# Kernel tuning notes

Measured on AMD Instinct MI355X. Metric: run time of the kernel, lower is better.

The kernel has to match this reference:

```python
import jax, jax.numpy as jnp
import numpy as np

N_NODES = 50000
IN_DIM = 128
HID = 128
N_EDGES = 1000000


def setup_inputs() -> dict:
    key = jax.random.key(0)
    k1, k2, k3, k4, k5, k6, k7 = jax.random.split(key, 7)
    patient_embeds = jax.random.normal(k1, (N_NODES, IN_DIM), dtype=jnp.float32)
    condition_embeds = jax.random.normal(k2, (N_NODES, IN_DIM), dtype=jnp.float32)
    edge_index = jax.random.randint(k3, (2, N_EDGES), 0, N_NODES, dtype=jnp.int64)
    # MLP params: Linear(2*IN_DIM -> HID), Linear(HID -> 1)
    s1 = 1.0 / np.sqrt(2 * IN_DIM)
    s2 = 1.0 / np.sqrt(HID)
    W1 = jax.random.uniform(k4, (2 * IN_DIM, HID), minval=-s1, maxval=s1, dtype=jnp.float32)
    b1 = jax.random.uniform(k5, (HID,), minval=-s1, maxval=s1, dtype=jnp.float32)
    W2 = jax.random.uniform(k6, (HID, 1), minval=-s2, maxval=s2, dtype=jnp.float32)
    b2 = jax.random.uniform(k7, (1,), minval=-s2, maxval=s2, dtype=jnp.float32)
    return {
        "patient_embeds": patient_embeds,
        "condition_embeds": condition_embeds,
        "edge_index": edge_index,
        "W1": W1, "b1": b1, "W2": W2, "b2": b2,
    }


def reference(patient_embeds, condition_embeds, edge_index, W1, b1, W2, b2):
    src = patient_embeds[edge_index[0]]        # [E, D]
    dst = condition_embeds[edge_index[1]]      # [E, D]
    # concat + first Linear == split-matmul; avoids materializing [E, 2D]
    h = src @ W1[:IN_DIM] + dst @ W1[IN_DIM:] + b1   # [E, HID]
    h = jax.nn.relu(h)
    logits = h @ W2 + b2                        # [E, 1]
    return jax.nn.sigmoid(logits).squeeze(-1)   # [E]
```

## Files before the change

kernel.cpp:

```cpp
#include <hip/hip_runtime.h>
#include <hip/hip_bf16.h>

#define IN_DIM   128
#define HIDDEN   128
#define KDIM     256
#define TILE_E   32
#define NTHREADS 512
#define LDBW     264

typedef __attribute__((ext_vector_type(8)))  short bf16x8;
typedef __attribute__((ext_vector_type(16))) float f32x16;

__device__ __forceinline__ unsigned short f2bf(float f) {
    union { __hip_bfloat16 h; unsigned short u; } cv;
    cv.h = __float2bfloat16(f);
    return cv.u;
}

__global__ void prep_kernel(const float* __restrict__ pat,
                            const float* __restrict__ cond,
                            const float* __restrict__ W1,
                            unsigned short* __restrict__ pat_bf,
                            unsigned short* __restrict__ cond_bf,
                            unsigned short* __restrict__ W1T,
                            int n_vec, int do_tables) {
    const int w1_units = HIDDEN * KDIM / 8;
    const long long total = do_tables ? (2LL * n_vec + w1_units) : w1_units;
    const long long stride = (long long)gridDim.x * blockDim.x;
    for (long long u = blockIdx.x * (long long)blockDim.x + threadIdx.x;
         u < total; u += stride) {
        if (do_tables && u < 2LL * n_vec) {
            int which = (u >= n_vec);
            long long v = which ? u - n_vec : u;
            const float* src = which ? cond : pat;
            unsigned short* dst = which ? cond_bf : pat_bf;
            long long base = v * 8;
            float4 x = *(const float4*)(src + base);
            float4 y = *(const float4*)(src + base + 4);
            unsigned short hv[8];
            hv[0]=f2bf(x.x); hv[1]=f2bf(x.y); hv[2]=f2bf(x.z); hv[3]=f2bf(x.w);
            hv[4]=f2bf(y.x); hv[5]=f2bf(y.y); hv[6]=f2bf(y.z); hv[7]=f2bf(y.w);
            *(uint4*)(dst + base) = *(uint4*)hv;
        } else {
            int idx = (int)(u - (do_tables ? 2LL * n_vec : 0));
            int c  = idx >> 5;
            int k0 = (idx & 31) * 8;
            unsigned short hv[8];
            #pragma unroll
            for (int j = 0; j < 8; ++j)
                hv[j] = f2bf(W1[(k0 + j) * HIDDEN + c]);
            *(uint4*)(W1T + c * KDIM + k0) = *(uint4*)hv;
        }
    }
}

__global__ __launch_bounds__(NTHREADS, 4)
void link_mlp_kernel(const float* __restrict__ pat,
                     const float* __restrict__ cond,
                     const unsigned short* __restrict__ tbl_p,
                     const unsigned short* __restrict__ tbl_c,
                     const int* __restrict__ eidx,
                     const unsigned short* __restrict__ W1T,
                     const float* __restrict__ b1,
                     const float* __restrict__ W2,
                     const float* __restrict__ b2,
                     float* __restrict__ out,
                     int E, int n_nodes, int ntiles)
{
    __shared__ unsigned short sB[HIDDEN * LDBW];
    __shared__ float sLog[8][TILE_E];

    const int t = threadIdx.x;

    #pragma unroll
    for (int it = 0; it < 8; ++it) {
        int ci = it * NTHREADS + t;
        int c = ci >> 5, j = ci & 31;
        *(uint4*)&sB[c * LDBW + j * 8] = *(const uint4*)(W1T + c * KDIM + j * 8);
    }
    __syncthreads();

    const int w    = t >> 6;
    const int lane = t & 63;
    const int c32  = lane & 31;
    const int hi   = lane >> 5;

    float b1v[4], w2v[4];
    #pragma unroll
    for (int nt = 0; nt < 4; ++nt) {
        int col = nt * 32 + c32;
        b1v[nt] = b1[col];
        w2v[nt] = W2[col];
    }
    const float b2v = b2[0];

    const int wslots = gridDim.x * (NTHREADS / 64);

    for (int tile = blockIdx.x * (NTHREADS / 64) + w; tile < ntiles; tile += wslots) {
        const int e  = tile * TILE_E + c32;
        const int eC = min(e, E - 1);
        int np = eidx[eC];     np = min(max(np, 0), n_nodes - 1);
        int nc = eidx[E + eC]; nc = min(max(nc, 0), n_nodes - 1);

        f32x16 acc[4];
        #pragma unroll
        for (int nt = 0; nt < 4; ++nt)
            acc[nt] = (f32x16){0.f,0.f,0.f,0.f,0.f,0.f,0.f,0.f,
                               0.f,0.f,0.f,0.f,0.f,0.f,0.f,0.f};

        if (tbl_p) {
            const unsigned short* bp = tbl_p + np * IN_DIM + hi * 8;
            const unsigned short* bc = tbl_c + nc * IN_DIM + hi * 8;
            #pragma unroll
            for (int ksb = 0; ksb < 4; ++ksb) {
                bf16x8 a[4];
                #pragma unroll
                for (int j = 0; j < 4; ++j) {
                    int ks = ksb * 4 + j;
                    const unsigned short* src =
                        (ks < 8) ? (bp + ks * 16) : (bc + (ks - 8) * 16);
                    a[j] = *(const bf16x8*)src;
                }
                #pragma unroll
                for (int j = 0; j < 4; ++j) {
                    int ks = ksb * 4 + j;
                    #pragma unroll
                    for (int nt = 0; nt < 4; ++nt) {
                        bf16x8 b = *(const bf16x8*)
                            &sB[(nt * 32 + c32) * LDBW + ks * 16 + hi * 8];
                        acc[nt] = __builtin_amdgcn_mfma_f32_32x32x16_bf16(
                            a[j], b, acc[nt], 0, 0, 0);
                    }
                }
            }
        } else {
            const float* fp = pat  + (long long)np * IN_DIM + hi * 8;
            const float* fc = cond + (long long)nc * IN_DIM + hi * 8;
            #pragma unroll
            for (int ksb = 0; ksb < 4; ++ksb) {
                bf16x8 a[4];
                #pragma unroll
                for (int j = 0; j < 4; ++j) {
                    int ks = ksb * 4 + j;
                    const float* src = (ks < 8) ? (fp + ks * 16) : (fc + (ks - 8) * 16);
                    float4 x = *(const float4*)src;
                    float4 y = *(const float4*)(src + 4);
                    unsigned short hv[8];
                    hv[0]=f2bf(x.x); hv[1]=f2bf(x.y); hv[2]=f2bf(x.z); hv[3]=f2bf(x.w);
                    hv[4]=f2bf(y.x); hv[5]=f2bf(y.y); hv[6]=f2bf(y.z); hv[7]=f2bf(y.w);
                    a[j] = *(bf16x8*)hv;
                }
                #pragma unroll
                for (int j = 0; j < 4; ++j) {
                    int ks = ksb * 4 + j;
                    #pragma unroll
                    for (int nt = 0; nt < 4; ++nt) {
                        bf16x8 b = *(const bf16x8*)
                            &sB[(nt * 32 + c32) * LDBW + ks * 16 + hi * 8];
                        acc[nt] = __builtin_amdgcn_mfma_f32_32x32x16_bf16(
                            a[j], b, acc[nt], 0, 0, 0);
                    }
                }
            }
        }

        float p[16];
        #pragma unroll
        for (int r = 0; r < 16; ++r) {
            float s = 0.f;
            #pragma unroll
            for (int nt = 0; nt < 4; ++nt)
                s += fmaxf(acc[nt][r] + b1v[nt], 0.f) * w2v[nt];
            p[r] = s;
        }
        #pragma unroll
        for (int off = 1; off < 32; off <<= 1)
            #pragma unroll
            for (int r = 0; r < 16; ++r)
                p[r] += __shfl_xor(p[r], off, 64);
        if (c32 == 0) {
            #pragma unroll
            for (int r = 0; r < 16; ++r)
                sLog[w][(r & 3) + 8 * (r >> 2) + 4 * hi] = p[r];
        }
        float x  = sLog[w][c32] + b2v;
        float sg = 1.f / (1.f + __expf(-x));
        if (hi == 0 && e < E) out[e] = sg;
    }
}

extern "C" void kernel_launch(void* const* d_in, const int* in_sizes, int n_in,
                              void* d_out, int out_size, void* d_ws, size_t ws_size,
                              hipStream_t stream) {
    const float* pat  = (const float*)d_in[0];
    const float* cond = (const float*)d_in[1];
    const int*   eidx = (const int*)d_in[2];
    const float* W1   = (const float*)d_in[3];
    const float* b1   = (const float*)d_in[4];
    const float* W2   = (const float*)d_in[5];
    const float* b2   = (const float*)d_in[6];
    float*       out  = (float*)d_out;

    const int E       = in_sizes[2] / 2;
    const int n_nodes = in_sizes[0] / IN_DIM;
    const int ntiles  = (E + TILE_E - 1) / TILE_E;

    unsigned short* W1T = (unsigned short*)d_ws;
    const size_t tbl_bytes = (size_t)n_nodes * IN_DIM * 2;
    unsigned short* pat_bf  = (unsigned short*)((char*)d_ws + 65536);
    unsigned short* cond_bf = (unsigned short*)((char*)d_ws + 65536 + tbl_bytes);
    const bool use_tbl = ws_size >= 65536 + 2 * tbl_bytes;

    const int n_vec = n_nodes * IN_DIM / 8;
    prep_kernel<<<2048, 256, 0, stream>>>(pat, cond, W1, pat_bf, cond_bf, W1T,
                                          n_vec, use_tbl ? 1 : 0);

    const int nblocks = 512;
    link_mlp_kernel<<<nblocks, NTHREADS, 0, stream>>>(
        pat, cond,
        use_tbl ? pat_bf : nullptr, use_tbl ? cond_bf : nullptr,
        eidx, W1T, b1, W2, b2, out, E, n_nodes, ntiles);
}
```

Baseline: 190.7 us.

## Software-pipeline gathers across tiles and use transpose-style shuffle reduction

Splits the bf16-table path into a dedicated kernel that prefetches the next tile's indices and patient rows while the current tile's MFMAs run, so gather latency is overlapped with compute. The cross-lane reduction is replaced with a butterfly that halves the live values at each step and writes outputs directly, removing the shared-memory logit buffer. Launch bounds drop to 2 blocks per CU to give room for the extra registers that hold prefetched fragments, which may lower occupancy.

```diff
diff --git a/kernel.cpp b/kernel.cpp
--- a/kernel.cpp
+++ b/kernel.cpp
@@ -54,10 +54,25 @@
     }
 }
 
-__global__ __launch_bounds__(NTHREADS, 4)
-void link_mlp_kernel(const float* __restrict__ pat,
-                     const float* __restrict__ cond,
-                     const unsigned short* __restrict__ tbl_p,
+#define LOADC(Ab, base, off)                                        \
+    { _Pragma("unroll")                                             \
+      for (int j = 0; j < 4; ++j)                                   \
+          Ab[j] = *(const bf16x8*)((base) + (off) + j * 16); }
+
+#define MFMA_CHUNK(Ab, ks0)                                         \
+    { _Pragma("unroll")                                             \
+      for (int j = 0; j < 4; ++j) {                                 \
+          const int ks = (ks0) + j;                                 \
+          _Pragma("unroll")                                         \
+          for (int nt = 0; nt < 4; ++nt) {                          \
+              bf16x8 bfrag = *(const bf16x8*)                       \
+                  &sB[(nt * 32 + c32) * LDBW + ks * 16 + hi * 8];   \
+              acc[nt] = __builtin_amdgcn_mfma_f32_32x32x16_bf16(    \
+                  Ab[j], bfrag, acc[nt], 0, 0, 0);                  \
+          } } }
+
+__global__ __launch_bounds__(NTHREADS, 2)
+void link_mlp_kernel(const unsigned short* __restrict__ tbl_p,
                      const unsigned short* __restrict__ tbl_c,
                      const int* __restrict__ eidx,
                      const unsigned short* __restrict__ W1T,
@@ -68,10 +83,8 @@
                      int E, int n_nodes, int ntiles)
 {
     __shared__ unsigned short sB[HIDDEN * LDBW];
-    __shared__ float sLog[8][TILE_E];
 
     const int t = threadIdx.x;
-
     #pragma unroll
     for (int it = 0; it < 8; ++it) {
         int ci = it * NTHREADS + t;
@@ -94,6 +107,147 @@
     }
     const float b2v = b2[0];
 
+    const int ws = gridDim.x * (NTHREADS / 64);
+    int tile = blockIdx.x * (NTHREADS / 64) + w;
+    if (tile >= ntiles) return;
+
+    const unsigned short* bcC;
+    bf16x8 A0[4], A1[4], A2[4], A3[4];
+    {
+        int eC = min(tile * TILE_E + c32, E - 1);
+        int npR = eidx[eC], ncR = eidx[E + eC];
+        int np = min(max(npR, 0), n_nodes - 1);
+        int nc = min(max(ncR, 0), n_nodes - 1);
+        const unsigned short* bpC = tbl_p + np * IN_DIM + hi * 8;
+        bcC = tbl_c + nc * IN_DIM + hi * 8;
+        LOADC(A0, bpC, 0);
+        LOADC(A1, bpC, 64);
+    }
+    int npN = 0, ncN = 0;
+    {
+        int tn = tile + ws;
+        if (tn < ntiles) {
+            int e2 = min(tn * TILE_E + c32, E - 1);
+            npN = eidx[e2]; ncN = eidx[E + e2];
+        }
+    }
+
+    while (true) {
+        LOADC(A2, bcC, 0);
+        LOADC(A3, bcC, 64);
+
+        f32x16 acc[4];
+        #pragma unroll
+        for (int nt = 0; nt < 4; ++nt)
+            acc[nt] = (f32x16){0.f,0.f,0.f,0.f,0.f,0.f,0.f,0.f,
+                               0.f,0.f,0.f,0.f,0.f,0.f,0.f,0.f};
+
+        MFMA_CHUNK(A0, 0);
+        MFMA_CHUNK(A1, 4);
+
+        const int tn = tile + ws;
+        const unsigned short* bcN;
+        {
+            int np = min(max(npN, 0), n_nodes - 1);
+            int nc = min(max(ncN, 0), n_nodes - 1);
+            const unsigned short* bpN = tbl_p + np * IN_DIM + hi * 8;
+            bcN = tbl_c + nc * IN_DIM + hi * 8;
+            if (tn < ntiles) {
+                LOADC(A0, bpN, 0);
+                LOADC(A1, bpN, 64);
+                int tnn = min(tn + ws, ntiles - 1);
+                int e3 = min(tnn * TILE_E + c32, E - 1);
+                npN = eidx[e3]; ncN = eidx[E + e3];
+            }
+        }
+
+        MFMA_CHUNK(A2, 8);
+        MFMA_CHUNK(A3, 12);
+
+        float v[16];
+        #pragma unroll
+        for (int r = 0; r < 16; ++r) {
+            float s = 0.f;
+            #pragma unroll
+            for (int nt = 0; nt < 4; ++nt)
+                s += fmaxf(acc[nt][r] + b1v[nt], 0.f) * w2v[nt];
+            v[r] = s;
+        }
+        #pragma unroll
+        for (int j = 0; j < 16; ++j) v[j] += __shfl_xor(v[j], 1, 64);
+        const bool bb0 = (lane & 1);
+        float w8[8];
+        #pragma unroll
+        for (int j = 0; j < 8; ++j) w8[j] = bb0 ? v[j + 8] : v[j];
+        #pragma unroll
+        for (int j = 0; j < 8; ++j) w8[j] += __shfl_xor(w8[j], 2, 64);
+        const bool bb1 = (lane >> 1) & 1;
+        float x4[4];
+        #pragma unroll
+        for (int j = 0; j < 4; ++j) x4[j] = bb1 ? w8[j + 4] : w8[j];
+        #pragma unroll
+        for (int j = 0; j < 4; ++j) x4[j] += __shfl_xor(x4[j], 4, 64);
+        const bool bb2 = (lane >> 2) & 1;
+        float y2[2];
+        #pragma unroll
+        for (int j = 0; j < 2; ++j) y2[j] = bb2 ? x4[j + 2] : x4[j];
+        #pragma unroll
+        for (int j = 0; j < 2; ++j) y2[j] += __shfl_xor(y2[j], 8, 64);
+        const bool bb3 = (lane >> 3) & 1;
+        float z = bb3 ? y2[1] : y2[0];
+        z += __shfl_xor(z, 16, 64);
+
+        {
+            int r = ((lane & 1) << 3) | (((lane >> 1) & 1) << 2) |
+                    (((lane >> 2) & 1) << 1) | ((lane >> 3) & 1);
+            int row = (r & 3) + ((r >> 2) << 3) + 4 * hi;
+            int erow = tile * TILE_E + row;
+            if (!(lane & 16) && erow < E)
+                out[erow] = 1.f / (1.f + __expf(-(z + b2v)));
+        }
+
+        if (tn >= ntiles) break;
+        bcC = bcN;
+        tile = tn;
+    }
+}
+
+__global__ __launch_bounds__(NTHREADS, 2)
+void link_mlp_f32_kernel(const float* __restrict__ pat,
+                         const float* __restrict__ cond,
+                         const int* __restrict__ eidx,
+                         const unsigned short* __restrict__ W1T,
+                         const float* __restrict__ b1,
+                         const float* __restrict__ W2,
+                         const float* __restrict__ b2,
+                         float* __restrict__ out,
+                         int E, int n_nodes, int ntiles)
+{
+    __shared__ unsigned short sB[HIDDEN * LDBW];
+    __shared__ float sLog[8][TILE_E];
+
+    const int t = threadIdx.x;
+    #pragma unroll
+    for (int it = 0; it < 8; ++it) {
+        int ci = it * NTHREADS + t;
+        int c = ci >> 5, j = ci & 31;
+        *(uint4*)&sB[c * LDBW + j * 8] = *(const uint4*)(W1T + c * KDIM + j * 8);
+    }
+    __syncthreads();
+
+    const int w    = t >> 6;
+    const int lane = t & 63;
+    const int c32  = lane & 31;
+    const int hi   = lane >> 5;
+
+    float b1v[4], w2v[4];
+    #pragma unroll
+    for (int nt = 0; nt < 4; ++nt) {
+        int col = nt * 32 + c32;
+        b1v[nt] = b1[col];
+        w2v[nt] = W2[col];
+    }
+    const float b2v = b2[0];
     const int wslots = gridDim.x * (NTHREADS / 64);
 
     for (int tile = blockIdx.x * (NTHREADS / 64) + w; tile < ntiles; tile += wslots) {
@@ -108,58 +262,31 @@
             acc[nt] = (f32x16){0.f,0.f,0.f,0.f,0.f,0.f,0.f,0.f,
                                0.f,0.f,0.f,0.f,0.f,0.f,0.f,0.f};
 
-        if (tbl_p) {
-            const unsigned short* bp = tbl_p + np * IN_DIM + hi * 8;
-            const unsigned short* bc = tbl_c + nc * IN_DIM + hi * 8;
-            #pragma unroll
-            for (int ksb = 0; ksb < 4; ++ksb) {
-                bf16x8 a[4];
+        const float* fp = pat  + (long long)np * IN_DIM + hi * 8;
+        const float* fc = cond + (long long)nc * IN_DIM + hi * 8;
+        #pragma unroll
+        for (int ksb = 0; ksb < 4; ++ksb) {
+            bf16x8 a[4];
+            #pragma unroll
+            for (int j = 0; j < 4; ++j) {
+                int ks = ksb * 4 + j;
+                const float* src = (ks < 8) ? (fp + ks * 16) : (fc + (ks - 8) * 16);
+                float4 x = *(const float4*)src;
+                float4 y = *(const float4*)(src + 4);
+                unsigned short hv[8];
+                hv[0]=f2bf(x.x); hv[1]=f2bf(x.y); hv[2]=f2bf(x.z); hv[3]=f2bf(x.w);
+                hv[4]=f2bf(y.x); hv[5]=f2bf(y.y); hv[6]=f2bf(y.z); hv[7]=f2bf(y.w);
+                a[j] = *(bf16x8*)hv;
+            }
+            #pragma unroll
+            for (int j = 0; j < 4; ++j) {
+                int ks = ksb * 4 + j;
                 #pragma unroll
-                for (int j = 0; j < 4; ++j) {
-                    int ks = ksb * 4 + j;
-                    const unsigned short* src =
-                        (ks < 8) ? (bp + ks * 16) : (bc + (ks - 8) * 16);
-                    a[j] = *(const bf16x8*)src;
-                }
-                #pragma unroll
-                for (int j = 0; j < 4; ++j) {
-                    int ks = ksb * 4 + j;
-                    #pragma unroll
-                    for (int nt = 0; nt < 4; ++nt) {
-                        bf16x8 b = *(const bf16x8*)
-                            &sB[(nt * 32 + c32) * LDBW + ks * 16 + hi * 8];
-                        acc[nt] = __builtin_amdgcn_mfma_f32_32x32x16_bf16(
-                            a[j], b, acc[nt], 0, 0, 0);
-                    }
-                }
-            }
-        } else {
-            const float* fp = pat  + (long long)np * IN_DIM + hi * 8;
-            const float* fc = cond + (long long)nc * IN_DIM + hi * 8;
-            #pragma unroll
-            for (int ksb = 0; ksb < 4; ++ksb) {
-                bf16x8 a[4];
-                #pragma unroll
-                for (int j = 0; j < 4; ++j) {
-                    int ks = ksb * 4 + j;
-                    const float* src = (ks < 8) ? (fp + ks * 16) : (fc + (ks - 8) * 16);
-                    float4 x = *(const float4*)src;
-                    float4 y = *(const float4*)(src + 4);
-                    unsigned short hv[8];
-                    hv[0]=f2bf(x.x); hv[1]=f2bf(x.y); hv[2]=f2bf(x.z); hv[3]=f2bf(x.w);
-                    hv[4]=f2bf(y.x); hv[5]=f2bf(y.y); hv[6]=f2bf(y.z); hv[7]=f2bf(y.w);
-                    a[j] = *(bf16x8*)hv;
-                }
-                #pragma unroll
-                for (int j = 0; j < 4; ++j) {
-                    int ks = ksb * 4 + j;
-                    #pragma unroll
-                    for (int nt = 0; nt < 4; ++nt) {
-                        bf16x8 b = *(const bf16x8*)
-                            &sB[(nt * 32 + c32) * LDBW + ks * 16 + hi * 8];
-                        acc[nt] = __builtin_amdgcn_mfma_f32_32x32x16_bf16(
-                            a[j], b, acc[nt], 0, 0, 0);
-                    }
+                for (int nt = 0; nt < 4; ++nt) {
+                    bf16x8 b = *(const bf16x8*)
+                        &sB[(nt * 32 + c32) * LDBW + ks * 16 + hi * 8];
+                    acc[nt] = __builtin_amdgcn_mfma_f32_32x32x16_bf16(
+                        a[j], b, acc[nt], 0, 0, 0);
                 }
             }
         }
@@ -216,8 +343,11 @@
                                           n_vec, use_tbl ? 1 : 0);
 
     const int nblocks = 512;
-    link_mlp_kernel<<<nblocks, NTHREADS, 0, stream>>>(
-        pat, cond,
-        use_tbl ? pat_bf : nullptr, use_tbl ? cond_bf : nullptr,
-        eidx, W1T, b1, W2, b2, out, E, n_nodes, ntiles);
-}
+    if (use_tbl) {
+        link_mlp_kernel<<<nblocks, NTHREADS, 0, stream>>>(
+            pat_bf, cond_bf, eidx, W1T, b1, W2, b2, out, E, n_nodes, ntiles);
+    } else {
+        link_mlp_f32_kernel<<<nblocks, NTHREADS, 0, stream>>>(
+            pat, cond, eidx, W1T, b1, W2, b2, out, E, n_nodes, ntiles);
+    }
+}
```

New measurement: 473.5 us. 2.48x slower.

## Precompute per-node hidden projections, then gather and sum per edge in slices

Applied to the files above, without the earlier changes.

The first linear layer is split algebraically. Each node's patient and condition rows are projected once through W1 with MFMA into bf16 hidden tables, replacing a 256-deep matmul on every edge. The edge pass then gathers 16-wide slices of the two projected rows, adds them, applies ReLU and a dot with W2, and writes bf16 partial sums per slice; a finalize kernel sums the slices and applies the sigmoid. This cuts the per-edge MFMA work, but adds an intermediate partial-sum buffer, an extra kernel launch, and bf16 rounding of both the hidden values and the partial sums.

```diff
diff --git a/kernel.cpp b/kernel.cpp
--- a/kernel.cpp
+++ b/kernel.cpp
@@ -4,9 +4,10 @@
 #define IN_DIM   128
 #define HIDDEN   128
 #define KDIM     256
-#define TILE_E   32
-#define NTHREADS 512
+#define NTH_G    512
 #define LDBW     264
+#define NSLICE   8
+#define SLICE_D  16
 
 typedef __attribute__((ext_vector_type(8)))  short bf16x8;
 typedef __attribute__((ext_vector_type(16))) float f32x16;
@@ -16,88 +17,199 @@
     cv.h = __float2bfloat16(f);
     return cv.u;
 }
-
-__global__ void prep_kernel(const float* __restrict__ pat,
-                            const float* __restrict__ cond,
-                            const float* __restrict__ W1,
-                            unsigned short* __restrict__ pat_bf,
-                            unsigned short* __restrict__ cond_bf,
-                            unsigned short* __restrict__ W1T,
-                            int n_vec, int do_tables) {
-    const int w1_units = HIDDEN * KDIM / 8;
-    const long long total = do_tables ? (2LL * n_vec + w1_units) : w1_units;
-    const long long stride = (long long)gridDim.x * blockDim.x;
-    for (long long u = blockIdx.x * (long long)blockDim.x + threadIdx.x;
-         u < total; u += stride) {
-        if (do_tables && u < 2LL * n_vec) {
-            int which = (u >= n_vec);
-            long long v = which ? u - n_vec : u;
-            const float* src = which ? cond : pat;
-            unsigned short* dst = which ? cond_bf : pat_bf;
-            long long base = v * 8;
-            float4 x = *(const float4*)(src + base);
-            float4 y = *(const float4*)(src + base + 4);
-            unsigned short hv[8];
-            hv[0]=f2bf(x.x); hv[1]=f2bf(x.y); hv[2]=f2bf(x.z); hv[3]=f2bf(x.w);
-            hv[4]=f2bf(y.x); hv[5]=f2bf(y.y); hv[6]=f2bf(y.z); hv[7]=f2bf(y.w);
-            *(uint4*)(dst + base) = *(uint4*)hv;
-        } else {
-            int idx = (int)(u - (do_tables ? 2LL * n_vec : 0));
-            int c  = idx >> 5;
-            int k0 = (idx & 31) * 8;
-            unsigned short hv[8];
-            #pragma unroll
-            for (int j = 0; j < 8; ++j)
-                hv[j] = f2bf(W1[(k0 + j) * HIDDEN + c]);
-            *(uint4*)(W1T + c * KDIM + k0) = *(uint4*)hv;
-        }
-    }
-}
-
-__global__ __launch_bounds__(NTHREADS, 4)
-void link_mlp_kernel(const float* __restrict__ pat,
-                     const float* __restrict__ cond,
-                     const unsigned short* __restrict__ tbl_p,
-                     const unsigned short* __restrict__ tbl_c,
-                     const int* __restrict__ eidx,
-                     const unsigned short* __restrict__ W1T,
-                     const float* __restrict__ b1,
-                     const float* __restrict__ W2,
-                     const float* __restrict__ b2,
-                     float* __restrict__ out,
-                     int E, int n_nodes, int ntiles)
+__device__ __forceinline__ float bf_lo(unsigned int v) { return __uint_as_float(v << 16); }
+__device__ __forceinline__ float bf_hi(unsigned int v) { return __uint_as_float(v & 0xffff0000u); }
+
+__global__ void w1t_kernel(const float* __restrict__ W1,
+                           unsigned short* __restrict__ W1T) {
+    int o = blockIdx.x * blockDim.x + threadIdx.x;
+    if (o >= HIDDEN * KDIM / 8) return;
+    int c = o >> 5;
+    int k0 = (o & 31) * 8;
+    unsigned short hv[8];
+    #pragma unroll
+    for (int j = 0; j < 8; ++j) hv[j] = f2bf(W1[(k0 + j) * HIDDEN + c]);
+    *(uint4*)(W1T + c * KDIM + k0) = *(uint4*)hv;
+}
+
+__global__ __launch_bounds__(NTH_G, 4)
+void hgemm_kernel(const float* __restrict__ pat,
+                  const float* __restrict__ cond,
+                  const unsigned short* __restrict__ W1T,
+                  const float* __restrict__ b1,
+                  unsigned short* __restrict__ hpS,
+                  unsigned short* __restrict__ hcS,
+                  int n_nodes)
 {
     __shared__ unsigned short sB[HIDDEN * LDBW];
-    __shared__ float sLog[8][TILE_E];
-
     const int t = threadIdx.x;
-
     #pragma unroll
     for (int it = 0; it < 8; ++it) {
-        int ci = it * NTHREADS + t;
+        int ci = it * NTH_G + t;
         int c = ci >> 5, j = ci & 31;
         *(uint4*)&sB[c * LDBW + j * 8] = *(const uint4*)(W1T + c * KDIM + j * 8);
     }
     __syncthreads();
 
-    const int w    = t >> 6;
-    const int lane = t & 63;
-    const int c32  = lane & 31;
-    const int hi   = lane >> 5;
-
-    float b1v[4], w2v[4];
+    const int w = t >> 6, lane = t & 63, c32 = lane & 31, hi = lane >> 5;
+    const int pass = w >> 2;
+    const int m    = w & 3;
+    const int nb   = blockIdx.x * 128 + m * 32;
+    if (nb >= n_nodes) return;
+
+    const float* tbl = pass ? cond : pat;
+    const int row = min(nb + c32, n_nodes - 1);
+
+    bf16x8 A[8];
+    #pragma unroll
+    for (int ks = 0; ks < 8; ++ks) {
+        const float* ap = tbl + (long long)row * IN_DIM + ks * 16 + hi * 8;
+        float4 x = *(const float4*)ap;
+        float4 y = *(const float4*)(ap + 4);
+        unsigned short hv[8];
+        hv[0]=f2bf(x.x); hv[1]=f2bf(x.y); hv[2]=f2bf(x.z); hv[3]=f2bf(x.w);
+        hv[4]=f2bf(y.x); hv[5]=f2bf(y.y); hv[6]=f2bf(y.z); hv[7]=f2bf(y.w);
+        A[ks] = *(bf16x8*)hv;
+    }
+
+    f32x16 acc[4];
+    #pragma unroll
+    for (int nt = 0; nt < 4; ++nt)
+        acc[nt] = (f32x16){0.f,0.f,0.f,0.f,0.f,0.f,0.f,0.f,
+                           0.f,0.f,0.f,0.f,0.f,0.f,0.f,0.f};
+    #pragma unroll
+    for (int ks = 0; ks < 8; ++ks)
+        #pragma unroll
+        for (int nt = 0; nt < 4; ++nt) {
+            bf16x8 b = *(const bf16x8*)
+                &sB[(nt * 32 + c32) * LDBW + pass * 128 + ks * 16 + hi * 8];
+            acc[nt] = __builtin_amdgcn_mfma_f32_32x32x16_bf16(A[ks], b, acc[nt], 0, 0, 0);
+        }
+
+    float b1v[4];
+    #pragma unroll
+    for (int nt = 0; nt < 4; ++nt) b1v[nt] = pass ? 0.f : b1[nt * 32 + c32];
+    unsigned short* dst = pass ? hcS : hpS;
+
     #pragma unroll
     for (int nt = 0; nt < 4; ++nt) {
         int col = nt * 32 + c32;
-        b1v[nt] = b1[col];
-        w2v[nt] = W2[col];
-    }
+        int sl = col >> 4, j = col & 15;
+        unsigned short* dcol = dst + (long long)sl * n_nodes * SLICE_D + j;
+        #pragma unroll
+        for (int r = 0; r < 16; ++r) {
+            int node = nb + (r & 3) + 8 * (r >> 2) + 4 * hi;
+            if (node < n_nodes)
+                dcol[(long long)node * SLICE_D] = f2bf(acc[nt][r] + b1v[nt]);
+        }
+    }
+}
+
+__global__ __launch_bounds__(256, 4)
+void edge_kernel(const unsigned short* __restrict__ hpS,
+                 const unsigned short* __restrict__ hcS,
+                 const int* __restrict__ eidx,
+                 const float* __restrict__ W2,
+                 unsigned short* __restrict__ part,
+                 int E, int n_nodes)
+{
+    const int slice = blockIdx.x & (NSLICE - 1);
+    const int bid2  = blockIdx.x >> 3;
+    const int lane  = threadIdx.x & 63;
+    const int w     = threadIdx.x >> 6;
+
+    float w2s[16];
+    #pragma unroll
+    for (int j = 0; j < 16; ++j) w2s[j] = W2[slice * SLICE_D + j];
+
+    const unsigned short* hs = hpS + (long long)slice * n_nodes * SLICE_D;
+    const unsigned short* hd = hcS + (long long)slice * n_nodes * SLICE_D;
+    unsigned short* ps = part + (long long)slice * E;
+
+    const int widS = bid2 * 4 + w;
+    const int nwS  = (gridDim.x >> 3) * 4;
+
+    for (long long base = (long long)widS * 64; base < E; base += (long long)nwS * 64) {
+        int e  = (int)base + lane;
+        int eC = min(e, E - 1);
+        int np = eidx[eC];     np = min(max(np, 0), n_nodes - 1);
+        int nc = eidx[E + eC]; nc = min(max(nc, 0), n_nodes - 1);
+
+        const uint4* sp = (const uint4*)(hs + (long long)np * SLICE_D);
+        const uint4* dp = (const uint4*)(hd + (long long)nc * SLICE_D);
+        uint4 s0 = sp[0], s1 = sp[1];
+        uint4 d0 = dp[0], d1 = dp[1];
+
+        unsigned int sa[8] = {s0.x, s0.y, s0.z, s0.w, s1.x, s1.y, s1.z, s1.w};
+        unsigned int da[8] = {d0.x, d0.y, d0.z, d0.w, d1.x, d1.y, d1.z, d1.w};
+        float p = 0.f;
+        #pragma unroll
+        for (int q = 0; q < 8; ++q) {
+            float hlo = fmaxf(bf_lo(sa[q]) + bf_lo(da[q]), 0.f);
+            float hhi = fmaxf(bf_hi(sa[q]) + bf_hi(da[q]), 0.f);
+            p += hlo * w2s[2 * q] + hhi * w2s[2 * q + 1];
+        }
+        if (e < E) ps[e] = f2bf(p);
+    }
+}
+
+__global__ __launch_bounds__(256)
+void finalize_kernel(const unsigned short* __restrict__ part,
+                     const float* __restrict__ b2,
+                     float* __restrict__ out, int E)
+{
     const float b2v = b2[0];
-
-    const int wslots = gridDim.x * (NTHREADS / 64);
-
-    for (int tile = blockIdx.x * (NTHREADS / 64) + w; tile < ntiles; tile += wslots) {
-        const int e  = tile * TILE_E + c32;
+    const int stride = gridDim.x * blockDim.x;
+    const int npair = (E + 1) >> 1;
+    for (int i = blockIdx.x * blockDim.x + threadIdx.x; i < npair; i += stride) {
+        int e0 = i * 2;
+        float s0 = 0.f, s1 = 0.f;
+        #pragma unroll
+        for (int sl = 0; sl < NSLICE; ++sl) {
+            const unsigned short* pp = part + (long long)sl * E + e0;
+            s0 += __uint_as_float(((unsigned int)pp[0]) << 16);
+            if (e0 + 1 < E) s1 += __uint_as_float(((unsigned int)pp[1]) << 16);
+        }
+        out[e0] = 1.f / (1.f + __expf(-(s0 + b2v)));
+        if (e0 + 1 < E) out[e0 + 1] = 1.f / (1.f + __expf(-(s1 + b2v)));
+    }
+}
+
+__global__ __launch_bounds__(NTH_G, 4)
+void link_mlp_f32_kernel(const float* __restrict__ pat,
+                         const float* __restrict__ cond,
+                         const int* __restrict__ eidx,
+                         const unsigned short* __restrict__ W1T,
+                         const float* __restrict__ b1,
+                         const float* __restrict__ W2,
+                         const float* __restrict__ b2,
+                         float* __restrict__ out,
+                         int E, int n_nodes, int ntiles)
+{
+    __shared__ unsigned short sB[HIDDEN * LDBW];
+    __shared__ float sLog[8][32];
+
+    const int t = threadIdx.x;
+    #pragma unroll
+    for (int it = 0; it < 8; ++it) {
+        int ci = it * NTH_G + t;
+        int c = ci >> 5, j = ci & 31;
+        *(uint4*)&sB[c * LDBW + j * 8] = *(const uint4*)(W1T + c * KDIM + j * 8);
+    }
+    __syncthreads();
+
+    const int w = t >> 6, lane = t & 63, c32 = lane & 31, hi = lane >> 5;
+    float b1v[4], w2v[4];
+    #pragma unroll
+    for (int nt = 0; nt < 4; ++nt) {
+        int col = nt * 32 + c32;
+        b1v[nt] = b1[col]; w2v[nt] = W2[col];
+    }
+    const float b2v = b2[0];
+    const int wslots = gridDim.x * (NTH_G / 64);
+
+    for (int tile = blockIdx.x * (NTH_G / 64) + w; tile < ntiles; tile += wslots) {
+        const int e  = tile * 32 + c32;
         const int eC = min(e, E - 1);
         int np = eidx[eC];     np = min(max(np, 0), n_nodes - 1);
         int nc = eidx[E + eC]; nc = min(max(nc, 0), n_nodes - 1);
@@ -108,58 +220,30 @@
             acc[nt] = (f32x16){0.f,0.f,0.f,0.f,0.f,0.f,0.f,0.f,
                                0.f,0.f,0.f,0.f,0.f,0.f,0.f,0.f};
 
-        if (tbl_p) {
-            const unsigned short* bp = tbl_p + np * IN_DIM + hi * 8;
-            const unsigned short* bc = tbl_c + nc * IN_DIM + hi * 8;
-            #pragma unroll
-            for (int ksb = 0; ksb < 4; ++ksb) {
-                bf16x8 a[4];
+        const float* fp = pat  + (long long)np * IN_DIM + hi * 8;
+        const float* fc = cond + (long long)nc * IN_DIM + hi * 8;
+        #pragma unroll
+        for (int ksb = 0; ksb < 4; ++ksb) {
+            bf16x8 a[4];
+            #pragma unroll
+            for (int j = 0; j < 4; ++j) {
+                int ks = ksb * 4 + j;
+                const float* src = (ks < 8) ? (fp + ks * 16) : (fc + (ks - 8) * 16);
+                float4 x = *(const float4*)src;
+                float4 y = *(const float4*)(src + 4);
+                unsigned short hv[8];
+                hv[0]=f2bf(x.x); hv[1]=f2bf(x.y); hv[2]=f2bf(x.z); hv[3]=f2bf(x.w);
+                hv[4]=f2bf(y.x); hv[5]=f2bf(y.y); hv[6]=f2bf(y.z); hv[7]=f2bf(y.w);
+                a[j] = *(bf16x8*)hv;
+            }
+            #pragma unroll
+            for (int j = 0; j < 4; ++j) {
+                int ks = ksb * 4 + j;
                 #pragma unroll
-                for (int j = 0; j < 4; ++j) {
-                    int ks = ksb * 4 + j;
-                    const unsigned short* src =
-                        (ks < 8) ? (bp + ks * 16) : (bc + (ks - 8) * 16);
-                    a[j] = *(const bf16x8*)src;
-                }
-                #pragma unroll
-                for (int j = 0; j < 4; ++j) {
-                    int ks = ksb * 4 + j;
-                    #pragma unroll
-                    for (int nt = 0; nt < 4; ++nt) {
-                        bf16x8 b = *(const bf16x8*)
-                            &sB[(nt * 32 + c32) * LDBW + ks * 16 + hi * 8];
-                        acc[nt] = __builtin_amdgcn_mfma_f32_32x32x16_bf16(
-                            a[j], b, acc[nt], 0, 0, 0);
-                    }
-                }
-            }
-        } else {
-            const float* fp = pat  + (long long)np * IN_DIM + hi * 8;
-            const float* fc = cond + (long long)nc * IN_DIM + hi * 8;
-            #pragma unroll
-            for (int ksb = 0; ksb < 4; ++ksb) {
-                bf16x8 a[4];
-                #pragma unroll
-                for (int j = 0; j < 4; ++j) {
-                    int ks = ksb * 4 + j;
-                    const float* src = (ks < 8) ? (fp + ks * 16) : (fc + (ks - 8) * 16);
-                    float4 x = *(const float4*)src;
-                    float4 y = *(const float4*)(src + 4);
-                    unsigned short hv[8];
-                    hv[0]=f2bf(x.x); hv[1]=f2bf(x.y); hv[2]=f2bf(x.z); hv[3]=f2bf(x.w);
-                    hv[4]=f2bf(y.x); hv[5]=f2bf(y.y); hv[6]=f2bf(y.z); hv[7]=f2bf(y.w);
-                    a[j] = *(bf16x8*)hv;
-                }
-                #pragma unroll
-                for (int j = 0; j < 4; ++j) {
-                    int ks = ksb * 4 + j;
-                    #pragma unroll
-                    for (int nt = 0; nt < 4; ++nt) {
-                        bf16x8 b = *(const bf16x8*)
-                            &sB[(nt * 32 + c32) * LDBW + ks * 16 + hi * 8];
-                        acc[nt] = __builtin_amdgcn_mfma_f32_32x32x16_bf16(
-                            a[j], b, acc[nt], 0, 0, 0);
-                    }
+                for (int nt = 0; nt < 4; ++nt) {
+                    bf16x8 b = *(const bf16x8*)
+                        &sB[(nt * 32 + c32) * LDBW + ks * 16 + hi * 8];
+                    acc[nt] = __builtin_amdgcn_mfma_f32_32x32x16_bf16(a[j], b, acc[nt], 0, 0, 0);
                 }
             }
         }
@@ -203,21 +287,25 @@
 
     const int E       = in_sizes[2] / 2;
     const int n_nodes = in_sizes[0] / IN_DIM;
-    const int ntiles  = (E + TILE_E - 1) / TILE_E;
 
     unsigned short* W1T = (unsigned short*)d_ws;
-    const size_t tbl_bytes = (size_t)n_nodes * IN_DIM * 2;
-    unsigned short* pat_bf  = (unsigned short*)((char*)d_ws + 65536);
-    unsigned short* cond_bf = (unsigned short*)((char*)d_ws + 65536 + tbl_bytes);
-    const bool use_tbl = ws_size >= 65536 + 2 * tbl_bytes;
-
-    const int n_vec = n_nodes * IN_DIM / 8;
-    prep_kernel<<<2048, 256, 0, stream>>>(pat, cond, W1, pat_bf, cond_bf, W1T,
-                                          n_vec, use_tbl ? 1 : 0);
-
-    const int nblocks = 512;
-    link_mlp_kernel<<<nblocks, NTHREADS, 0, stream>>>(
-        pat, cond,
-        use_tbl ? pat_bf : nullptr, use_tbl ? cond_bf : nullptr,
-        eidx, W1T, b1, W2, b2, out, E, n_nodes, ntiles);
-}
+    const size_t tblB  = (size_t)n_nodes * HIDDEN * 2;
+    const size_t partB = (size_t)NSLICE * E * 2;
+    unsigned short* hpS  = (unsigned short*)((char*)d_ws + 65536);
+    unsigned short* hcS  = (unsigned short*)((char*)d_ws + 65536 + tblB);
+    unsigned short* prt  = (unsigned short*)((char*)d_ws + 65536 + 2 * tblB);
+    const bool use_new = ws_size >= 65536 + 2 * tblB + partB;
+
+    w1t_kernel<<<16, 256, 0, stream>>>(W1, W1T);
+
+    if (use_new) {
+        hgemm_kernel<<<(n_nodes + 127) / 128, NTH_G, 0, stream>>>(
+            pat, cond, W1T, b1, hpS, hcS, n_nodes);
+        edge_kernel<<<2048, 256, 0, stream>>>(hpS, hcS, eidx, W2, prt, E, n_nodes);
+        finalize_kernel<<<1024, 256, 0, stream>>>(prt, b2, out, E);
+    } else {
+        const int ntiles = (E + 31) / 32;
+        link_mlp_f32_kernel<<<512, NTH_G, 0, stream>>>(
+            pat, cond, eidx, W1T, b1, W2, b2, out, E, n_nodes, ntiles);
+    }
+}
```

After: 201.6 us. 1.06x slower.
